# Kernel optimization log

Hardware: AMD Instinct MI355X
Metric: run time of the kernel (lower is better)

## Reference

```python
import jax, jax.numpy as jnp
import numpy as np

B, M, NH, EH = 16, 128, 256, 128


def setup_inputs() -> dict:
    key = jax.random.key(0)
    ks = jax.random.split(key, 10)
    s = 0.05
    return {
        "X": jax.random.normal(ks[0], (B, M, NH), dtype=jnp.float32),
        "E": jax.random.normal(ks[1], (B, M, M, EH), dtype=jnp.float32),
        "A": jax.random.uniform(ks[2], (B, M, M), dtype=jnp.float32),
        "w": jax.random.uniform(ks[3], (B, M, 1), dtype=jnp.float32),
        "Wv_w": jax.random.normal(ks[4], (NH, NH), dtype=jnp.float32) * s,
        "Wv_b": jnp.zeros((NH,), dtype=jnp.float32),
        "We_w": jax.random.normal(ks[5], (EH, EH), dtype=jnp.float32) * s,
        "We_b": jnp.zeros((EH,), dtype=jnp.float32),
        "Wu_w": jax.random.normal(ks[6], (2 * NH + EH, NH), dtype=jnp.float32) * s,
        "Wu_b": jnp.zeros((NH,), dtype=jnp.float32),
    }


def reference(X, E, A, w, Wv_w, Wv_b, We_w, We_b, Wu_w, Wu_b):
    act = jax.nn.relu
    # W_v / W_e single-layer FFNs (capacity=0 -> one Linear)
    node_map = X @ Wv_w + Wv_b                      # [B, m, nh]
    edge_map = E @ We_w + We_b                      # [B, m, m, eh]
    # Fused aggregation: sum_i A[b,i,j] * cat(node_map[b,i], edge_map[b,i,j])
    # (avoids materializing the [B,m,m,nh+eh] intermediate; same math)
    agg_node = jnp.einsum('bij,bid->bjd', A, node_map)   # [B, m, nh]
    agg_edge = jnp.einsum('bij,bije->bje', A, edge_map)  # [B, m, eh]
    h = jnp.concatenate([agg_node, agg_edge, X], axis=2) # [B, m, 2nh+eh]
    out = (act(h) @ Wu_w + Wu_b) * w                     # [B, m, nh]
    return out
```

## Files before the change

### kernel.cpp

```cpp
#include <hip/hip_runtime.h>

namespace {

constexpr int Bn   = 16;
constexpr int Mn   = 128;
constexpr int NHn  = 256;
constexpr int EHn  = 128;
constexpr int ROWS = Bn * Mn;
constexpr int HW   = 2 * NHn + EHn;

constexpr int HP = HW + 4;
constexpr int AP = NHn + 4;
constexpr int TP = EHn + 4;

__device__ __forceinline__ float4 f4zero() { return make_float4(0.f, 0.f, 0.f, 0.f); }

__device__ __forceinline__ void f4fma(float4& acc, float a, const float4& v) {
    acc.x = fmaf(a, v.x, acc.x);
    acc.y = fmaf(a, v.y, acc.y);
    acc.z = fmaf(a, v.z, acc.z);
    acc.w = fmaf(a, v.w, acc.w);
}

__device__ __forceinline__ float4 f4add(const float4& a, const float4& b) {
    return make_float4(a.x + b.x, a.y + b.y, a.z + b.z, a.w + b.w);
}

__device__ __forceinline__ float4 f4relu(const float4& a) {
    return make_float4(fmaxf(a.x, 0.f), fmaxf(a.y, 0.f),
                       fmaxf(a.z, 0.f), fmaxf(a.w, 0.f));
}

__global__ __launch_bounds__(256) void k_reduce(
    const float* __restrict__ E, const float* __restrict__ A,
    const float* __restrict__ X,
    float* __restrict__ T, float* __restrict__ AX, float* __restrict__ CS)
{
    const int bid = blockIdx.x;
    const int b   = bid >> 7;
    const int j   = bid & (Mn - 1);
    const int tid = threadIdx.x;
    const int wv  = tid >> 6;

    __shared__ float  acol[Mn];
    __shared__ float4 tbuf[4][32];
    __shared__ float  abuf[4];
    __shared__ float4 axbuf[4][64];

    const float* Acol = A + (size_t)b * Mn * Mn + j;
    const float* Eb   = E + (size_t)b * Mn * Mn * EHn + (size_t)j * EHn;

    if (tid < Mn) acol[tid] = Acol[(size_t)tid * Mn];
    __syncthreads();

    {
        const int g  = tid >> 5;
        const int f4 = tid & 31;
        float4 acc = f4zero();
        float  as  = 0.f;
        #pragma unroll
        for (int it = 0; it < 16; ++it) {
            const int   i = it * 8 + g;
            const float a = acol[i];
            const float4 e4 = *reinterpret_cast<const float4*>(
                Eb + (size_t)i * (Mn * EHn) + f4 * 4);
            f4fma(acc, a, e4);
            as += a;
        }
        acc.x += __shfl_xor(acc.x, 32);
        acc.y += __shfl_xor(acc.y, 32);
        acc.z += __shfl_xor(acc.z, 32);
        acc.w += __shfl_xor(acc.w, 32);
        as    += __shfl_xor(as, 32);
        if ((tid & 63) < 32) tbuf[wv][f4] = acc;
        if ((tid & 63) == 0) abuf[wv] = as;
    }

    {
        const int d4 = tid & 63;
        float4 ax = f4zero();
        #pragma unroll 4
        for (int it = 0; it < 32; ++it) {
            const int   i = it * 4 + wv;
            const float a = acol[i];
            const float4 x4 = *reinterpret_cast<const float4*>(
                X + (size_t)(b * Mn + i) * NHn + d4 * 4);
            f4fma(ax, a, x4);
        }
        axbuf[wv][d4] = ax;
    }
    __syncthreads();

    if (tid < 32) {
        float4 s = f4add(f4add(tbuf[0][tid], tbuf[1][tid]),
                         f4add(tbuf[2][tid], tbuf[3][tid]));
        *reinterpret_cast<float4*>(T + (size_t)bid * EHn + tid * 4) = s;
    }
    if (tid == 0) {
        CS[bid] = abuf[0] + abuf[1] + abuf[2] + abuf[3];
    }
    if (tid < 64) {
        float4 s = f4add(f4add(axbuf[0][tid], axbuf[1][tid]),
                         f4add(axbuf[2][tid], axbuf[3][tid]));
        *reinterpret_cast<float4*>(AX + (size_t)bid * NHn + tid * 4) = s;
    }
}

__global__ __launch_bounds__(256) void k_mix(
    const float* __restrict__ AX, const float* __restrict__ T,
    const float* __restrict__ CS, const float* __restrict__ X,
    const float* __restrict__ Wv, const float* __restrict__ Wvb,
    const float* __restrict__ We, const float* __restrict__ Web,
    const float* __restrict__ Wu, const float* __restrict__ Wub,
    const float* __restrict__ wrow, float* __restrict__ out)
{
    const int r0  = blockIdx.x * 8;
    const int tid = threadIdx.x;

    __shared__ float axs[8][AP];
    __shared__ float ts[8][TP];
    __shared__ float hs[8][HP];
    __shared__ float csb[8];

    #pragma unroll
    for (int p = 0; p < 2; ++p) {
        const int idx = p * 256 + tid;
        const int r = idx >> 6, c = idx & 63;
        *reinterpret_cast<float4*>(&axs[r][c * 4]) =
            *reinterpret_cast<const float4*>(AX + (size_t)(r0 + r) * NHn + c * 4);
    }
    {
        const int r = tid >> 5, c = tid & 31;
        *reinterpret_cast<float4*>(&ts[r][c * 4]) =
            *reinterpret_cast<const float4*>(T + (size_t)(r0 + r) * EHn + c * 4);
    }
    #pragma unroll
    for (int p = 0; p < 2; ++p) {
        const int idx = p * 256 + tid;
        const int r = idx >> 6, c = idx & 63;
        const float4 x4 = *reinterpret_cast<const float4*>(
            X + (size_t)(r0 + r) * NHn + c * 4);
        *reinterpret_cast<float4*>(&hs[r][NHn + EHn + c * 4]) = f4relu(x4);
    }
    if (tid < 8) csb[tid] = CS[r0 + tid];
    __syncthreads();

    {
        const int rg = tid >> 6;
        const int c4 = tid & 63;
        const int ra = 2 * rg, rb = ra + 1;
        float4 a0 = f4zero(), a1 = f4zero();
        #pragma unroll 2
        for (int k = 0; k < NHn; k += 4) {
            const float4 h4a = *reinterpret_cast<const float4*>(&axs[ra][k]);
            const float4 h4b = *reinterpret_cast<const float4*>(&axs[rb][k]);
            const float* wp = Wv + (size_t)k * NHn + c4 * 4;
            const float4 w0 = *reinterpret_cast<const float4*>(wp);
            const float4 w1 = *reinterpret_cast<const float4*>(wp + NHn);
            const float4 w2 = *reinterpret_cast<const float4*>(wp + 2 * NHn);
            const float4 w3 = *reinterpret_cast<const float4*>(wp + 3 * NHn);
            f4fma(a0, h4a.x, w0); f4fma(a1, h4b.x, w0);
            f4fma(a0, h4a.y, w1); f4fma(a1, h4b.y, w1);
            f4fma(a0, h4a.z, w2); f4fma(a1, h4b.z, w2);
            f4fma(a0, h4a.w, w3); f4fma(a1, h4b.w, w3);
        }
        const float4 bv = *reinterpret_cast<const float4*>(Wvb + c4 * 4);
        f4fma(a0, csb[ra], bv);
        f4fma(a1, csb[rb], bv);
        *reinterpret_cast<float4*>(&hs[ra][c4 * 4]) = f4relu(a0);
        *reinterpret_cast<float4*>(&hs[rb][c4 * 4]) = f4relu(a1);
    }
    {
        const int er = tid >> 5;
        const int ec = tid & 31;
        float4 a = f4zero();
        #pragma unroll 2
        for (int k = 0; k < EHn; k += 4) {
            const float4 t4 = *reinterpret_cast<const float4*>(&ts[er][k]);
            const float* wp = We + (size_t)k * EHn + ec * 4;
            const float4 w0 = *reinterpret_cast<const float4*>(wp);
            const float4 w1 = *reinterpret_cast<const float4*>(wp + EHn);
            const float4 w2 = *reinterpret_cast<const float4*>(wp + 2 * EHn);
            const float4 w3 = *reinterpret_cast<const float4*>(wp + 3 * EHn);
            f4fma(a, t4.x, w0);
            f4fma(a, t4.y, w1);
            f4fma(a, t4.z, w2);
            f4fma(a, t4.w, w3);
        }
        const float4 be = *reinterpret_cast<const float4*>(Web + ec * 4);
        f4fma(a, csb[er], be);
        *reinterpret_cast<float4*>(&hs[er][NHn + ec * 4]) = f4relu(a);
    }
    __syncthreads();

    {
        const int rg = tid >> 6;
        const int c4 = tid & 63;
        const int ra = 2 * rg, rb = ra + 1;
        float4 a0 = f4zero(), a1 = f4zero();
        #pragma unroll 2
        for (int k = 0; k < HW; k += 4) {
            const float4 h4a = *reinterpret_cast<const float4*>(&hs[ra][k]);
            const float4 h4b = *reinterpret_cast<const float4*>(&hs[rb][k]);
            const float* wp = Wu + (size_t)k * NHn + c4 * 4;
            const float4 w0 = *reinterpret_cast<const float4*>(wp);
            const float4 w1 = *reinterpret_cast<const float4*>(wp + NHn);
            const float4 w2 = *reinterpret_cast<const float4*>(wp + 2 * NHn);
            const float4 w3 = *reinterpret_cast<const float4*>(wp + 3 * NHn);
            f4fma(a0, h4a.x, w0); f4fma(a1, h4b.x, w0);
            f4fma(a0, h4a.y, w1); f4fma(a1, h4b.y, w1);
            f4fma(a0, h4a.z, w2); f4fma(a1, h4b.z, w2);
            f4fma(a0, h4a.w, w3); f4fma(a1, h4b.w, w3);
        }
        const float4 bu = *reinterpret_cast<const float4*>(Wub + c4 * 4);
        const float w0 = wrow[r0 + ra], w1 = wrow[r0 + rb];
        float4 o0, o1;
        o0.x = (a0.x + bu.x) * w0;  o0.y = (a0.y + bu.y) * w0;
        o0.z = (a0.z + bu.z) * w0;  o0.w = (a0.w + bu.w) * w0;
        o1.x = (a1.x + bu.x) * w1;  o1.y = (a1.y + bu.y) * w1;
        o1.z = (a1.z + bu.z) * w1;  o1.w = (a1.w + bu.w) * w1;
        *reinterpret_cast<float4*>(out + (size_t)(r0 + ra) * NHn + c4 * 4) = o0;
        *reinterpret_cast<float4*>(out + (size_t)(r0 + rb) * NHn + c4 * 4) = o1;
    }
}

}

extern "C" void kernel_launch(void* const* d_in, const int* in_sizes, int n_in,
                              void* d_out, int out_size, void* d_ws, size_t ws_size,
                              hipStream_t stream) {
    const float* X   = (const float*)d_in[0];
    const float* E   = (const float*)d_in[1];
    const float* A   = (const float*)d_in[2];
    const float* w   = (const float*)d_in[3];
    const float* Wv  = (const float*)d_in[4];
    const float* Wvb = (const float*)d_in[5];
    const float* We  = (const float*)d_in[6];
    const float* Web = (const float*)d_in[7];
    const float* Wu  = (const float*)d_in[8];
    const float* Wub = (const float*)d_in[9];
    float* out = (float*)d_out;

    float* ws = (float*)d_ws;
    float* T  = ws;
    float* AX = T  + (size_t)ROWS * EHn;
    float* CS = AX + (size_t)ROWS * NHn;

    k_reduce<<<ROWS, 256, 0, stream>>>(E, A, X, T, AX, CS);
    k_mix<<<ROWS / 8, 256, 0, stream>>>(AX, T, CS, X, Wv, Wvb, We, Web,
                                        Wu, Wub, w, out);
}
```

Measured before the change: 288.3 us.

## Move A^T·X aggregation into mix kernel and split-K GEMMs across 512 threads

The reduce kernel now handles only the edge aggregation, with each block covering 4 output columns using float2 loads. The node aggregation (A^T X) and the column sums of A move into the mix kernel. That kernel now runs 512 threads, and each GEMM is split over K between two thread halves that are combined through shared memory. Weight loads are double-buffered in registers. This removes the AX/CS workspace round trip and raises parallelism in the mix stage, at the cost of extra syncs and redundant reads of A and X across blocks.

```diff
diff --git a/kernel.cpp b/kernel.cpp
--- a/kernel.cpp
+++ b/kernel.cpp
@@ -14,213 +14,252 @@
 constexpr int TP = EHn + 4;
 
 __device__ __forceinline__ float4 f4zero() { return make_float4(0.f, 0.f, 0.f, 0.f); }
-
+__device__ __forceinline__ float4 ld4(const float* p) {
+    return *reinterpret_cast<const float4*>(p);
+}
 __device__ __forceinline__ void f4fma(float4& acc, float a, const float4& v) {
     acc.x = fmaf(a, v.x, acc.x);
     acc.y = fmaf(a, v.y, acc.y);
     acc.z = fmaf(a, v.z, acc.z);
     acc.w = fmaf(a, v.w, acc.w);
 }
-
 __device__ __forceinline__ float4 f4add(const float4& a, const float4& b) {
     return make_float4(a.x + b.x, a.y + b.y, a.z + b.z, a.w + b.w);
 }
-
 __device__ __forceinline__ float4 f4relu(const float4& a) {
     return make_float4(fmaxf(a.x, 0.f), fmaxf(a.y, 0.f),
                        fmaxf(a.z, 0.f), fmaxf(a.w, 0.f));
 }
 
+#define LOADW(B, wb, ldw, kk) {                                        \
+    const float* _wp = (wb) + (size_t)(kk) * (ldw);                    \
+    B[0] = ld4(_wp);                 B[1] = ld4(_wp + (ldw));          \
+    B[2] = ld4(_wp + 2 * (ldw));     B[3] = ld4(_wp + 3 * (ldw)); }
+
+#define FMA2R(B, kk, opA, opB) {                                       \
+    const float4 _ha = ld4(&(opA)[kk]);                                \
+    const float4 _hb = ld4(&(opB)[kk]);                                \
+    f4fma(a0, _ha.x, B[0]); f4fma(a1, _hb.x, B[0]);                    \
+    f4fma(a0, _ha.y, B[1]); f4fma(a1, _hb.y, B[1]);                    \
+    f4fma(a0, _ha.z, B[2]); f4fma(a1, _hb.z, B[2]);                    \
+    f4fma(a0, _ha.w, B[3]); f4fma(a1, _hb.w, B[3]); }
+
+#define FMA1R(B, kk, opA) {                                            \
+    const float4 _ha = ld4(&(opA)[kk]);                                \
+    f4fma(a0, _ha.x, B[0]); f4fma(a0, _ha.y, B[1]);                    \
+    f4fma(a0, _ha.z, B[2]); f4fma(a0, _ha.w, B[3]); }
+
 __global__ __launch_bounds__(256) void k_reduce(
     const float* __restrict__ E, const float* __restrict__ A,
-    const float* __restrict__ X,
-    float* __restrict__ T, float* __restrict__ AX, float* __restrict__ CS)
+    float* __restrict__ T)
 {
     const int bid = blockIdx.x;
-    const int b   = bid >> 7;
-    const int j   = bid & (Mn - 1);
+    const int b   = bid >> 5;
+    const int j0  = (bid & 31) * 4;
     const int tid = threadIdx.x;
-    const int wv  = tid >> 6;
-
-    __shared__ float  acol[Mn];
-    __shared__ float4 tbuf[4][32];
-    __shared__ float  abuf[4];
-    __shared__ float4 axbuf[4][64];
-
-    const float* Acol = A + (size_t)b * Mn * Mn + j;
-    const float* Eb   = E + (size_t)b * Mn * Mn * EHn + (size_t)j * EHn;
-
-    if (tid < Mn) acol[tid] = Acol[(size_t)tid * Mn];
+
+    __shared__ float acolT[4][Mn];
+
+    if (tid < Mn) {
+        const float4 a4 = ld4(A + (size_t)b * Mn * Mn + (size_t)tid * Mn + j0);
+        acolT[0][tid] = a4.x; acolT[1][tid] = a4.y;
+        acolT[2][tid] = a4.z; acolT[3][tid] = a4.w;
+    }
     __syncthreads();
 
-    {
-        const int g  = tid >> 5;
-        const int f4 = tid & 31;
-        float4 acc = f4zero();
-        float  as  = 0.f;
-        #pragma unroll
-        for (int it = 0; it < 16; ++it) {
-            const int   i = it * 8 + g;
-            const float a = acol[i];
-            const float4 e4 = *reinterpret_cast<const float4*>(
-                Eb + (size_t)i * (Mn * EHn) + f4 * 4);
-            f4fma(acc, a, e4);
-            as += a;
-        }
-        acc.x += __shfl_xor(acc.x, 32);
-        acc.y += __shfl_xor(acc.y, 32);
-        acc.z += __shfl_xor(acc.z, 32);
-        acc.w += __shfl_xor(acc.w, 32);
-        as    += __shfl_xor(as, 32);
-        if ((tid & 63) < 32) tbuf[wv][f4] = acc;
-        if ((tid & 63) == 0) abuf[wv] = as;
-    }
-
-    {
-        const int d4 = tid & 63;
-        float4 ax = f4zero();
-        #pragma unroll 4
-        for (int it = 0; it < 32; ++it) {
-            const int   i = it * 4 + wv;
-            const float a = acol[i];
-            const float4 x4 = *reinterpret_cast<const float4*>(
-                X + (size_t)(b * Mn + i) * NHn + d4 * 4);
-            f4fma(ax, a, x4);
-        }
-        axbuf[wv][d4] = ax;
-    }
-    __syncthreads();
-
-    if (tid < 32) {
-        float4 s = f4add(f4add(tbuf[0][tid], tbuf[1][tid]),
-                         f4add(tbuf[2][tid], tbuf[3][tid]));
-        *reinterpret_cast<float4*>(T + (size_t)bid * EHn + tid * 4) = s;
-    }
-    if (tid == 0) {
-        CS[bid] = abuf[0] + abuf[1] + abuf[2] + abuf[3];
-    }
-    if (tid < 64) {
-        float4 s = f4add(f4add(axbuf[0][tid], axbuf[1][tid]),
-                         f4add(axbuf[2][tid], axbuf[3][tid]));
-        *reinterpret_cast<float4*>(AX + (size_t)bid * NHn + tid * 4) = s;
-    }
-}
-
-__global__ __launch_bounds__(256) void k_mix(
-    const float* __restrict__ AX, const float* __restrict__ T,
-    const float* __restrict__ CS, const float* __restrict__ X,
+    const int jj = tid >> 6;
+    const int f2 = tid & 63;
+    const float* Eb = E + (size_t)b * Mn * Mn * EHn + (size_t)(j0 + jj) * EHn
+                        + f2 * 2;
+    const float* ac = acolT[jj];
+
+    float2 acc = make_float2(0.f, 0.f);
+    #pragma unroll 16
+    for (int i = 0; i < Mn; ++i) {
+        const float2 e2 = *reinterpret_cast<const float2*>(
+            Eb + (size_t)i * (Mn * EHn));
+        const float a = ac[i];
+        acc.x = fmaf(a, e2.x, acc.x);
+        acc.y = fmaf(a, e2.y, acc.y);
+    }
+
+    const int row = b * Mn + j0 + jj;
+    *reinterpret_cast<float2*>(T + (size_t)row * EHn + f2 * 2) = acc;
+}
+
+__global__ __launch_bounds__(512, 2) void k_mix(
+    const float* __restrict__ T, const float* __restrict__ A,
+    const float* __restrict__ X,
     const float* __restrict__ Wv, const float* __restrict__ Wvb,
     const float* __restrict__ We, const float* __restrict__ Web,
     const float* __restrict__ Wu, const float* __restrict__ Wub,
     const float* __restrict__ wrow, float* __restrict__ out)
 {
     const int r0  = blockIdx.x * 8;
+    const int b   = r0 >> 7;
+    const int j0  = r0 & 127;
     const int tid = threadIdx.x;
 
-    __shared__ float axs[8][AP];
-    __shared__ float ts[8][TP];
-    __shared__ float hs[8][HP];
-    __shared__ float csb[8];
-
-    #pragma unroll
-    for (int p = 0; p < 2; ++p) {
-        const int idx = p * 256 + tid;
-        const int r = idx >> 6, c = idx & 63;
-        *reinterpret_cast<float4*>(&axs[r][c * 4]) =
-            *reinterpret_cast<const float4*>(AX + (size_t)(r0 + r) * NHn + c * 4);
-    }
-    {
+    __shared__ float  asl[Mn][8];
+    __shared__ float  ts[8][TP];
+    __shared__ float  axs[8][AP];
+    __shared__ float  hs[8][HP];
+    __shared__ float4 comb[256][2];
+    __shared__ float  pcs[8][8];
+    __shared__ float  csb[8];
+
+    {
+        const int i = tid >> 2, q = tid & 3;
+        const float2 a2 = *reinterpret_cast<const float2*>(
+            A + (size_t)b * Mn * Mn + (size_t)i * Mn + j0 + q * 2);
+        asl[i][q * 2]     = a2.x;
+        asl[i][q * 2 + 1] = a2.y;
+    }
+    if (tid < 256) {
         const int r = tid >> 5, c = tid & 31;
         *reinterpret_cast<float4*>(&ts[r][c * 4]) =
-            *reinterpret_cast<const float4*>(T + (size_t)(r0 + r) * EHn + c * 4);
-    }
-    #pragma unroll
-    for (int p = 0; p < 2; ++p) {
-        const int idx = p * 256 + tid;
-        const int r = idx >> 6, c = idx & 63;
-        const float4 x4 = *reinterpret_cast<const float4*>(
-            X + (size_t)(r0 + r) * NHn + c * 4);
-        *reinterpret_cast<float4*>(&hs[r][NHn + EHn + c * 4]) = f4relu(x4);
-    }
-    if (tid < 8) csb[tid] = CS[r0 + tid];
+            ld4(T + (size_t)(r0 + r) * EHn + c * 4);
+    }
+    {
+        const int r = tid >> 6, c4 = tid & 63;
+        const float4 x4 = ld4(X + (size_t)(r0 + r) * NHn + c4 * 4);
+        *reinterpret_cast<float4*>(&hs[r][NHn + EHn + c4 * 4]) = f4relu(x4);
+    }
     __syncthreads();
 
-    {
-        const int rg = tid >> 6;
-        const int c4 = tid & 63;
-        const int ra = 2 * rg, rb = ra + 1;
+    const int t8 = tid & 255;
+    const int rg = t8 >> 6;
+    const int c4 = t8 & 63;
+    const int kh = tid >> 8;
+    const int ra = 2 * rg, rb = ra + 1;
+
+    if (tid < 64) {
+        const int r = tid >> 3, seg = tid & 7;
+        float s = 0.f;
+        #pragma unroll
+        for (int i = 0; i < 16; ++i) s += asl[seg * 16 + i][r];
+        pcs[r][seg] = s;
+    }
+
+    {
+        const float* wb = X + (size_t)(b * Mn) * NHn + c4 * 4;
+        const int k0 = kh * 64;
+        float4 B0[4], B1[4];
         float4 a0 = f4zero(), a1 = f4zero();
-        #pragma unroll 2
-        for (int k = 0; k < NHn; k += 4) {
-            const float4 h4a = *reinterpret_cast<const float4*>(&axs[ra][k]);
-            const float4 h4b = *reinterpret_cast<const float4*>(&axs[rb][k]);
-            const float* wp = Wv + (size_t)k * NHn + c4 * 4;
-            const float4 w0 = *reinterpret_cast<const float4*>(wp);
-            const float4 w1 = *reinterpret_cast<const float4*>(wp + NHn);
-            const float4 w2 = *reinterpret_cast<const float4*>(wp + 2 * NHn);
-            const float4 w3 = *reinterpret_cast<const float4*>(wp + 3 * NHn);
-            f4fma(a0, h4a.x, w0); f4fma(a1, h4b.x, w0);
-            f4fma(a0, h4a.y, w1); f4fma(a1, h4b.y, w1);
-            f4fma(a0, h4a.z, w2); f4fma(a1, h4b.z, w2);
-            f4fma(a0, h4a.w, w3); f4fma(a1, h4b.w, w3);
-        }
-        const float4 bv = *reinterpret_cast<const float4*>(Wvb + c4 * 4);
-        f4fma(a0, csb[ra], bv);
-        f4fma(a1, csb[rb], bv);
-        *reinterpret_cast<float4*>(&hs[ra][c4 * 4]) = f4relu(a0);
-        *reinterpret_cast<float4*>(&hs[rb][c4 * 4]) = f4relu(a1);
-    }
-    {
+        LOADW(B0, wb, NHn, k0);
+        for (int k = k0; k < k0 + 64; k += 8) {
+            LOADW(B1, wb, NHn, k + 4);
+            {
+                const float4 _b = B0[0];
+                (void)_b;
+            }
+            {
+                f4fma(a0, asl[k    ][ra], B0[0]); f4fma(a1, asl[k    ][rb], B0[0]);
+                f4fma(a0, asl[k + 1][ra], B0[1]); f4fma(a1, asl[k + 1][rb], B0[1]);
+                f4fma(a0, asl[k + 2][ra], B0[2]); f4fma(a1, asl[k + 2][rb], B0[2]);
+                f4fma(a0, asl[k + 3][ra], B0[3]); f4fma(a1, asl[k + 3][rb], B0[3]);
+            }
+            if (k + 8 < k0 + 64) LOADW(B0, wb, NHn, k + 8);
+            {
+                f4fma(a0, asl[k + 4][ra], B1[0]); f4fma(a1, asl[k + 4][rb], B1[0]);
+                f4fma(a0, asl[k + 5][ra], B1[1]); f4fma(a1, asl[k + 5][rb], B1[1]);
+                f4fma(a0, asl[k + 6][ra], B1[2]); f4fma(a1, asl[k + 6][rb], B1[2]);
+                f4fma(a0, asl[k + 7][ra], B1[3]); f4fma(a1, asl[k + 7][rb], B1[3]);
+            }
+        }
+        if (kh == 1) { comb[t8][0] = a0; comb[t8][1] = a1; }
+        __syncthreads();
+        if (kh == 0) {
+            a0 = f4add(a0, comb[t8][0]);
+            a1 = f4add(a1, comb[t8][1]);
+            *reinterpret_cast<float4*>(&axs[ra][c4 * 4]) = a0;
+            *reinterpret_cast<float4*>(&axs[rb][c4 * 4]) = a1;
+        }
+        if (tid < 8) {
+            float s = 0.f;
+            #pragma unroll
+            for (int g = 0; g < 8; ++g) s += pcs[tid][g];
+            csb[tid] = s;
+        }
+        __syncthreads();
+    }
+
+    if (tid < 256) {
         const int er = tid >> 5;
         const int ec = tid & 31;
-        float4 a = f4zero();
-        #pragma unroll 2
-        for (int k = 0; k < EHn; k += 4) {
-            const float4 t4 = *reinterpret_cast<const float4*>(&ts[er][k]);
-            const float* wp = We + (size_t)k * EHn + ec * 4;
-            const float4 w0 = *reinterpret_cast<const float4*>(wp);
-            const float4 w1 = *reinterpret_cast<const float4*>(wp + EHn);
-            const float4 w2 = *reinterpret_cast<const float4*>(wp + 2 * EHn);
-            const float4 w3 = *reinterpret_cast<const float4*>(wp + 3 * EHn);
-            f4fma(a, t4.x, w0);
-            f4fma(a, t4.y, w1);
-            f4fma(a, t4.z, w2);
-            f4fma(a, t4.w, w3);
-        }
-        const float4 be = *reinterpret_cast<const float4*>(Web + ec * 4);
-        f4fma(a, csb[er], be);
-        *reinterpret_cast<float4*>(&hs[er][NHn + ec * 4]) = f4relu(a);
-    }
-    __syncthreads();
-
-    {
-        const int rg = tid >> 6;
-        const int c4 = tid & 63;
-        const int ra = 2 * rg, rb = ra + 1;
+        const float* wb = We + ec * 4;
+        const float* opA = ts[er];
+        float4 B0[4], B1[4];
+        float4 a0 = f4zero();
+        LOADW(B0, wb, EHn, 0);
+        for (int k = 0; k < EHn; k += 8) {
+            LOADW(B1, wb, EHn, k + 4);
+            FMA1R(B0, k, opA);
+            if (k + 8 < EHn) LOADW(B0, wb, EHn, k + 8);
+            FMA1R(B1, k + 4, opA);
+        }
+        const float4 be = ld4(Web + ec * 4);
+        f4fma(a0, csb[er], be);
+        *reinterpret_cast<float4*>(&hs[er][NHn + ec * 4]) = f4relu(a0);
+    }
+
+    {
+        const float* wb = Wv + c4 * 4;
+        const float* opA = axs[ra];
+        const float* opB = axs[rb];
+        const int k0 = kh * 128;
+        float4 B0[4], B1[4];
         float4 a0 = f4zero(), a1 = f4zero();
-        #pragma unroll 2
-        for (int k = 0; k < HW; k += 4) {
-            const float4 h4a = *reinterpret_cast<const float4*>(&hs[ra][k]);
-            const float4 h4b = *reinterpret_cast<const float4*>(&hs[rb][k]);
-            const float* wp = Wu + (size_t)k * NHn + c4 * 4;
-            const float4 w0 = *reinterpret_cast<const float4*>(wp);
-            const float4 w1 = *reinterpret_cast<const float4*>(wp + NHn);
-            const float4 w2 = *reinterpret_cast<const float4*>(wp + 2 * NHn);
-            const float4 w3 = *reinterpret_cast<const float4*>(wp + 3 * NHn);
-            f4fma(a0, h4a.x, w0); f4fma(a1, h4b.x, w0);
-            f4fma(a0, h4a.y, w1); f4fma(a1, h4b.y, w1);
-            f4fma(a0, h4a.z, w2); f4fma(a1, h4b.z, w2);
-            f4fma(a0, h4a.w, w3); f4fma(a1, h4b.w, w3);
-        }
-        const float4 bu = *reinterpret_cast<const float4*>(Wub + c4 * 4);
-        const float w0 = wrow[r0 + ra], w1 = wrow[r0 + rb];
-        float4 o0, o1;
-        o0.x = (a0.x + bu.x) * w0;  o0.y = (a0.y + bu.y) * w0;
-        o0.z = (a0.z + bu.z) * w0;  o0.w = (a0.w + bu.w) * w0;
-        o1.x = (a1.x + bu.x) * w1;  o1.y = (a1.y + bu.y) * w1;
-        o1.z = (a1.z + bu.z) * w1;  o1.w = (a1.w + bu.w) * w1;
-        *reinterpret_cast<float4*>(out + (size_t)(r0 + ra) * NHn + c4 * 4) = o0;
-        *reinterpret_cast<float4*>(out + (size_t)(r0 + rb) * NHn + c4 * 4) = o1;
+        LOADW(B0, wb, NHn, k0);
+        for (int k = k0; k < k0 + 128; k += 8) {
+            LOADW(B1, wb, NHn, k + 4);
+            FMA2R(B0, k, opA, opB);
+            if (k + 8 < k0 + 128) LOADW(B0, wb, NHn, k + 8);
+            FMA2R(B1, k + 4, opA, opB);
+        }
+        if (kh == 1) { comb[t8][0] = a0; comb[t8][1] = a1; }
+        __syncthreads();
+        if (kh == 0) {
+            a0 = f4add(a0, comb[t8][0]);
+            a1 = f4add(a1, comb[t8][1]);
+            const float4 bv = ld4(Wvb + c4 * 4);
+            f4fma(a0, csb[ra], bv);
+            f4fma(a1, csb[rb], bv);
+            *reinterpret_cast<float4*>(&hs[ra][c4 * 4]) = f4relu(a0);
+            *reinterpret_cast<float4*>(&hs[rb][c4 * 4]) = f4relu(a1);
+        }
+        __syncthreads();
+    }
+
+    {
+        const float* wb = Wu + c4 * 4;
+        const float* opA = hs[ra];
+        const float* opB = hs[rb];
+        const int k0 = kh * 320;
+        float4 B0[4], B1[4];
+        float4 a0 = f4zero(), a1 = f4zero();
+        LOADW(B0, wb, NHn, k0);
+        for (int k = k0; k < k0 + 320; k += 8) {
+            LOADW(B1, wb, NHn, k + 4);
+            FMA2R(B0, k, opA, opB);
+            if (k + 8 < k0 + 320) LOADW(B0, wb, NHn, k + 8);
+            FMA2R(B1, k + 4, opA, opB);
+        }
+        if (kh == 1) { comb[t8][0] = a0; comb[t8][1] = a1; }
+        __syncthreads();
+        if (kh == 0) {
+            a0 = f4add(a0, comb[t8][0]);
+            a1 = f4add(a1, comb[t8][1]);
+            const float4 bu = ld4(Wub + c4 * 4);
+            const float w0 = wrow[r0 + ra], w1 = wrow[r0 + rb];
+            float4 o0, o1;
+            o0.x = (a0.x + bu.x) * w0;  o0.y = (a0.y + bu.y) * w0;
+            o0.z = (a0.z + bu.z) * w0;  o0.w = (a0.w + bu.w) * w0;
+            o1.x = (a1.x + bu.x) * w1;  o1.y = (a1.y + bu.y) * w1;
+            o1.z = (a1.z + bu.z) * w1;  o1.w = (a1.w + bu.w) * w1;
+            *reinterpret_cast<float4*>(out + (size_t)(r0 + ra) * NHn + c4 * 4) = o0;
+            *reinterpret_cast<float4*>(out + (size_t)(r0 + rb) * NHn + c4 * 4) = o1;
+        }
     }
 }
 
@@ -241,12 +280,8 @@
     const float* Wub = (const float*)d_in[9];
     float* out = (float*)d_out;
 
-    float* ws = (float*)d_ws;
-    float* T  = ws;
-    float* AX = T  + (size_t)ROWS * EHn;
-    float* CS = AX + (size_t)ROWS * NHn;
-
-    k_reduce<<<ROWS, 256, 0, stream>>>(E, A, X, T, AX, CS);
-    k_mix<<<ROWS / 8, 256, 0, stream>>>(AX, T, CS, X, Wv, Wvb, We, Web,
-                                        Wu, Wub, w, out);
-}
+    float* T = (float*)d_ws;
+
+    k_reduce<<<512, 256, 0, stream>>>(E, A, T);
+    k_mix<<<256, 512, 0, stream>>>(T, A, X, Wv, Wvb, We, Web, Wu, Wub, w, out);
+}
```

Result: faster. 260.3 us (-9.7%).
